# Performance work log

Measured on AMD Instinct MI355X. Metric: run time of the kernel, lower is better.

## Reference

```python
import jax, jax.numpy as jnp
import numpy as np


def setup_inputs() -> dict:
    key = jax.random.key(0)
    k1, k2 = jax.random.split(key)
    N, D, K = 262144, 64, 1024
    residual = jax.random.normal(k1, (N, D), dtype=jnp.float32)
    # nn.init.uniform_(codebook.weight, -1/K, 1/K)
    codebook = jax.random.uniform(k2, (K, D), dtype=jnp.float32,
                                  minval=-1.0 / K, maxval=1.0 / K)
    return {"residual": residual, "codebook": codebook}


def reference(residual, codebook):
    # squared L2 distances via ||a||^2 + ||b||^2 - 2 a.b (argmin-equivalent to
    # the broadcast (N,K,D) form, without materializing it)
    r2 = jnp.sum(residual * residual, axis=1, keepdims=True)        # (N, 1)
    c2 = jnp.sum(codebook * codebook, axis=1)[None, :]              # (1, K)
    dists = r2 + c2 - 2.0 * (residual @ codebook.T)                 # (N, K)
    codes = jnp.argmin(dists, axis=1)                               # (N,) int
    quantized = codebook[codes]                                     # (N, D)
    return quantized, codes
```

## Files before the change

kernel.cpp:

```cpp
#include <hip/hip_runtime.h>
#include <float.h>

#define D 64

typedef float f32x4 __attribute__((ext_vector_type(4)));
typedef _Float16 f16x8 __attribute__((ext_vector_type(8)));

__device__ __forceinline__ float np_sum_sq_64(const float* v) {
  float s[8];
#pragma unroll
  for (int j = 0; j < 8; ++j) s[j] = __fmul_rn(v[j], v[j]);
#pragma unroll
  for (int b = 1; b < 8; ++b) {
#pragma unroll
    for (int j = 0; j < 8; ++j)
      s[j] = __fadd_rn(s[j], __fmul_rn(v[8 * b + j], v[8 * b + j]));
  }
  float t01 = __fadd_rn(s[0], s[1]);
  float t23 = __fadd_rn(s[2], s[3]);
  float t45 = __fadd_rn(s[4], s[5]);
  float t67 = __fadd_rn(s[6], s[7]);
  return __fadd_rn(__fadd_rn(t01, t23), __fadd_rn(t45, t67));
}

__device__ __forceinline__ unsigned int pkh(float a, float b) {
  union { _Float16 h[2]; unsigned int u; } x;
  x.h[0] = (_Float16)a;
  x.h[1] = (_Float16)b;
  return x.u;
}

__global__ __launch_bounds__(64) void vq_prep(
    const float* __restrict__ cb, unsigned short* __restrict__ cbh,
    float4* __restrict__ cbT4, float* __restrict__ c2,
    unsigned int* __restrict__ counters, int K) {
  if (blockIdx.x == 0 && threadIdx.x == 0) { counters[0] = 0u; counters[1] = 0u; }
  int k = blockIdx.x * 64 + threadIdx.x;
  if (k >= K) return;
  float row[D];
  const float4* cp = (const float4*)(cb + (size_t)k * D);
#pragma unroll
  for (int i = 0; i < 16; ++i) {
    float4 v = cp[i];
    row[4 * i] = v.x; row[4 * i + 1] = v.y;
    row[4 * i + 2] = v.z; row[4 * i + 3] = v.w;
    cbT4[(size_t)i * K + k] = v;
    *(uint2*)(cbh + (size_t)k * D + 4 * i) =
        make_uint2(pkh(v.x * 1024.f, v.y * 1024.f),
                   pkh(v.z * 1024.f, v.w * 1024.f));
  }
  c2[k] = np_sum_sq_64(row);
}

__global__ __launch_bounds__(256, 3) void vq_screen(
    const float* __restrict__ residual, const float* __restrict__ codebook,
    const unsigned short* __restrict__ cbh, const float* __restrict__ c2,
    float* __restrict__ out_q, float* __restrict__ codes_f,
    unsigned int* __restrict__ counters, int* __restrict__ list,
    int N, int K) {
  __shared__ unsigned short smem[4096];
  __shared__ float srow[64];

  int tid = threadIdx.x;
  int rowbase = blockIdx.x * 64;

  float sr4[4];
#pragma unroll
  for (int jj = 0; jj < 4; ++jj) {
    int i = tid + 256 * jj;
    int r = i >> 4, d0 = (i & 15) * 4;
    float4 v = *(const float4*)(residual + (size_t)(rowbase + r) * D + d0);
    sr4[jj] = fabsf(v.x) + fabsf(v.y) + fabsf(v.z) + fabsf(v.w);
    int tile = r >> 4, rr = r & 15;
    int kblk = d0 >> 5, kk = d0 & 31;
    int lanep = rr + 16 * (kk >> 3);
    int off = ((tile * 2 + kblk) * 64 + lanep) * 8 + (kk & 7);
    *(uint2*)(smem + off) = make_uint2(pkh(v.x, v.y), pkh(v.z, v.w));
  }
#pragma unroll
  for (int jj = 0; jj < 4; ++jj) {
    float s = sr4[jj];
    s += __shfl_xor(s, 1, 64);
    s += __shfl_xor(s, 2, 64);
    s += __shfl_xor(s, 4, 64);
    s += __shfl_xor(s, 8, 64);
    sr4[jj] = s;
  }
  if ((tid & 15) == 0) {
#pragma unroll
    for (int jj = 0; jj < 4; ++jj) srow[(tid >> 4) + 16 * jj] = sr4[jj];
  }
  __syncthreads();

  int w = tid >> 6, lane = tid & 63;
  int lane15 = lane & 15, lq = lane >> 4;

  f16x8 ah[4][2];
#pragma unroll
  for (int t = 0; t < 4; ++t)
#pragma unroll
    for (int kb = 0; kb < 2; ++kb)
      ah[t][kb] = *(const f16x8*)(smem + ((t * 2 + kb) * 64 + lane) * 8);

  float m1[4][4], m2[4][4], m3[4][4];
#pragma unroll
  for (int t = 0; t < 4; ++t)
#pragma unroll
    for (int j = 0; j < 4; ++j) {
      m1[t][j] = FLT_MAX; m2[t][j] = FLT_MAX; m3[t][j] = FLT_MAX;
    }

  const unsigned short* ph = cbh + (size_t)(w * 16 + lane15) * D + lq * 8;
  const float* pc2 = c2 + (w * 16 + lane15);

  f16x8 B0a = *(const f16x8*)(ph);
  f16x8 B1a = *(const f16x8*)(ph + 32);
  float c2a = *pc2;
  ph += 64 * D; pc2 += 64;
  f16x8 B0b = *(const f16x8*)(ph);
  f16x8 B1b = *(const f16x8*)(ph + 32);
  float c2b = *pc2;

  unsigned int idb = (unsigned int)((w << 4) | lane15);
  for (int cc = 0; cc < 16; ++cc) {
    f16x8 ch0 = B0a, ch1 = B1a;
    float c2v = c2a;
    B0a = B0b; B1a = B1b; c2a = c2b;
    if (cc < 14) {
      ph += 64 * D; pc2 += 64;
      B0b = *(const f16x8*)(ph);
      B1b = *(const f16x8*)(ph + 32);
      c2b = *pc2;
    }

#pragma unroll
    for (int t = 0; t < 4; ++t) {
      f32x4 a = {0.f, 0.f, 0.f, 0.f};
      a = __builtin_amdgcn_mfma_f32_16x16x32_f16(ah[t][0], ch0, a, 0, 0, 0);
      a = __builtin_amdgcn_mfma_f32_16x16x32_f16(ah[t][1], ch1, a, 0, 0, 0);
#pragma unroll
      for (int j = 0; j < 4; ++j) {
        float s = __builtin_fmaf(-0.001953125f, a[j], c2v);
        float spf = __uint_as_float((__float_as_uint(s) & 0xFFFFFC00u) | idb);
        float o2 = m2[t][j];
        m3[t][j] = __builtin_amdgcn_fmed3f(o2, m3[t][j], spf);
        m2[t][j] = __builtin_amdgcn_fmed3f(m1[t][j], o2, spf);
        m1[t][j] = fminf(m1[t][j], spf);
      }
    }
    idb += 64u;
  }

#pragma unroll
  for (int dlt = 1; dlt < 16; dlt <<= 1) {
#pragma unroll
    for (int t = 0; t < 4; ++t)
#pragma unroll
      for (int j = 0; j < 4; ++j) {
        float a1 = m1[t][j], a2 = m2[t][j], a3 = m3[t][j];
        float b1 = __shfl_xor(a1, dlt, 64);
        float b2 = __shfl_xor(a2, dlt, 64);
        float b3 = __shfl_xor(a3, dlt, 64);
        m1[t][j] = fminf(a1, b1);
        m2[t][j] = fminf(fminf(fmaxf(a1, b1), a2), b2);
        m3[t][j] = fminf(fminf(fmaxf(a2, b1), fmaxf(a1, b2)), fminf(a3, b3));
      }
  }

  __syncthreads();
  float* red = (float*)smem;
  int* code_lds = ((int*)smem) + 768;
  if (lane15 == 0) {
#pragma unroll
    for (int t = 0; t < 4; ++t)
#pragma unroll
      for (int j = 0; j < 4; ++j) {
        int r = t * 16 + lq * 4 + j;
        int base = (w * 64 + r) * 3;
        red[base + 0] = m1[t][j];
        red[base + 1] = m2[t][j];
        red[base + 2] = m3[t][j];
      }
  }
  __syncthreads();
  if (tid < 64) {
    float a1 = red[tid * 3 + 0], a2 = red[tid * 3 + 1], a3 = red[tid * 3 + 2];
#pragma unroll
    for (int wv = 1; wv < 4; ++wv) {
      float b1 = red[(wv * 64 + tid) * 3 + 0];
      float b2 = red[(wv * 64 + tid) * 3 + 1];
      float b3 = red[(wv * 64 + tid) * 3 + 2];
      float n1 = fminf(a1, b1);
      float n2 = fminf(fminf(fmaxf(a1, b1), a2), b2);
      float n3 = fminf(fminf(fmaxf(a2, b1), fmaxf(a1, b2)), fminf(a3, b3));
      a1 = n1; a2 = n2; a3 = n3;
    }
    unsigned int u1 = __float_as_uint(a1);
    unsigned int u2 = __float_as_uint(a2);
    unsigned int u3 = __float_as_uint(a3);
    int ka = (int)(u1 & 1023u);
    float g1 = __uint_as_float(u1 & 0xFFFFFC00u);
    float g2 = __uint_as_float(u2 & 0xFFFFFC00u);
    float g3 = __uint_as_float(u3 & 0xFFFFFC00u);
    float margin = __builtin_fmaf(srow[tid], 4.6e-6f, 4.0e-5f);
    int row = rowbase + tid;
    code_lds[tid] = ka;
    float cf = (float)ka;
    if (g2 - g1 < margin) {
      if (g3 - g1 < margin) {
        unsigned int s = atomicAdd(counters + 0, 1u);
        list[s] = row;
      } else {
        unsigned int s = atomicAdd(counters + 1, 1u);
        list[N - 1 - (int)s] = row;
        cf = (float)(int)((unsigned int)ka | ((u2 & 1023u) << 10));
      }
    }
    codes_f[row] = cf;
  }
  __syncthreads();

  for (int e = tid; e < 4096; e += 256) {
    int r = e >> 6, d = e & 63;
    out_q[(size_t)rowbase * D + e] = codebook[((size_t)code_lds[r] << 6) + d];
  }
}

__global__ __launch_bounds__(256) void vq_pair(
    const float* __restrict__ residual, const float* __restrict__ codebook,
    const float* __restrict__ c2, float* __restrict__ codes_f,
    float* __restrict__ out_q, const unsigned int* __restrict__ counters,
    const int* __restrict__ list, int N) {
  unsigned int cnt = counters[1];
  for (unsigned int i = blockIdx.x * 256 + threadIdx.x; i < cnt;
       i += gridDim.x * 256) {
    int row = list[N - 1 - (int)i];
    int packed = (int)codes_f[row];
    int ka = packed & 1023, kb = packed >> 10;

    float r[D];
    const float4* rp = (const float4*)(residual + ((size_t)row << 6));
#pragma unroll
    for (int q = 0; q < 16; ++q) {
      float4 v = rp[q];
      r[4 * q] = v.x; r[4 * q + 1] = v.y; r[4 * q + 2] = v.z; r[4 * q + 3] = v.w;
    }
    float r2 = np_sum_sq_64(r);

    float da = 0.f, db = 0.f;
    const float4* ap = (const float4*)(codebook + ((size_t)ka << 6));
    const float4* bp = (const float4*)(codebook + ((size_t)kb << 6));
#pragma unroll
    for (int q = 0; q < 16; ++q) {
      float4 x = ap[q], y = bp[q];
      da = __fmaf_rn(r[4 * q + 0], x.x, da); db = __fmaf_rn(r[4 * q + 0], y.x, db);
      da = __fmaf_rn(r[4 * q + 1], x.y, da); db = __fmaf_rn(r[4 * q + 1], y.y, db);
      da = __fmaf_rn(r[4 * q + 2], x.z, da); db = __fmaf_rn(r[4 * q + 2], y.z, db);
      da = __fmaf_rn(r[4 * q + 3], x.w, da); db = __fmaf_rn(r[4 * q + 3], y.w, db);
    }
    float dista = __fsub_rn(__fadd_rn(r2, c2[ka]), __fmul_rn(2.0f, da));
    float distb = __fsub_rn(__fadd_rn(r2, c2[kb]), __fmul_rn(2.0f, db));
    bool bwin = (distb < dista) || (distb == dista && kb < ka);
    int win = bwin ? kb : ka;
    codes_f[row] = (float)win;
    if (bwin) {
      float4* oq = (float4*)(out_q + ((size_t)row << 6));
      const float4* cw = (const float4*)(codebook + ((size_t)win << 6));
#pragma unroll
      for (int q = 0; q < 16; ++q) oq[q] = cw[q];
    }
  }
}

__global__ __launch_bounds__(256) void vq_rescore(
    const float* __restrict__ residual, const float* __restrict__ codebook,
    const float4* __restrict__ cbT4, const float* __restrict__ c2,
    float* __restrict__ codes_f, float* __restrict__ out_q,
    const unsigned int* __restrict__ counters,
    const int* __restrict__ list, int K) {
  unsigned int cnt = counters[0];
  int w = threadIdx.x >> 6, lane = threadIdx.x & 63;
  unsigned int npairs = (cnt + 1) >> 1;
  for (unsigned int g = blockIdx.x * 4 + w; g < npairs; g += gridDim.x * 4) {
    int n0 = list[2 * g];
    bool two = (2 * g + 1 < cnt);
    int n1 = two ? list[2 * g + 1] : n0;

    float rl0 = residual[(size_t)n0 * D + lane];
    float rl1 = residual[(size_t)n1 * D + lane];

    int j = lane & 7;
    float x0 = __shfl(rl0, j, 64), x1 = __shfl(rl1, j, 64);
    float s0 = __fmul_rn(x0, x0), s1 = __fmul_rn(x1, x1);
#pragma unroll
    for (int b = 1; b < 8; ++b) {
      x0 = __shfl(rl0, 8 * b + j, 64);
      x1 = __shfl(rl1, 8 * b + j, 64);
      s0 = __fadd_rn(s0, __fmul_rn(x0, x0));
      s1 = __fadd_rn(s1, __fmul_rn(x1, x1));
    }
    s0 = __fadd_rn(s0, __shfl_xor(s0, 1, 64));
    s1 = __fadd_rn(s1, __shfl_xor(s1, 1, 64));
    s0 = __fadd_rn(s0, __shfl_xor(s0, 2, 64));
    s1 = __fadd_rn(s1, __shfl_xor(s1, 2, 64));
    s0 = __fadd_rn(s0, __shfl_xor(s0, 4, 64));
    s1 = __fadd_rn(s1, __shfl_xor(s1, 4, 64));
    float r2_0 = s0, r2_1 = s1;

    float m0[16], m1v[16];
#pragma unroll
    for (int ch = 0; ch < 16; ++ch) { m0[ch] = 0.f; m1v[ch] = 0.f; }

    for (int d4 = 0; d4 < 16; ++d4) {
      float a0 = __shfl(rl0, 4 * d4, 64), b0 = __shfl(rl0, 4 * d4 + 1, 64);
      float c0 = __shfl(rl0, 4 * d4 + 2, 64), e0 = __shfl(rl0, 4 * d4 + 3, 64);
      float a1 = __shfl(rl1, 4 * d4, 64), b1 = __shfl(rl1, 4 * d4 + 1, 64);
      float c1 = __shfl(rl1, 4 * d4 + 2, 64), e1 = __shfl(rl1, 4 * d4 + 3, 64);
      const float4* bp = cbT4 + (size_t)d4 * K + lane;
      float4 cbv[8];
#pragma unroll
      for (int h = 0; h < 2; ++h) {
#pragma unroll
        for (int q = 0; q < 8; ++q) cbv[q] = bp[(h * 8 + q) * 64];
#pragma unroll
        for (int q = 0; q < 8; ++q) {
          int ch = h * 8 + q;
          float4 c = cbv[q];
          float t0 = m0[ch], t1 = m1v[ch];
          t0 = __fmaf_rn(a0, c.x, t0); t1 = __fmaf_rn(a1, c.x, t1);
          t0 = __fmaf_rn(b0, c.y, t0); t1 = __fmaf_rn(b1, c.y, t1);
          t0 = __fmaf_rn(c0, c.z, t0); t1 = __fmaf_rn(c1, c.z, t1);
          t0 = __fmaf_rn(e0, c.w, t0); t1 = __fmaf_rn(e1, c.w, t1);
          m0[ch] = t0; m1v[ch] = t1;
        }
      }
    }

    float best0 = FLT_MAX, best1 = FLT_MAX;
    int bk0 = 0, bk1 = 0;
#pragma unroll
    for (int ch = 0; ch < 16; ++ch) {
      int code = ch * 64 + lane;
      float c2v = c2[code];
      float d0 = __fsub_rn(__fadd_rn(r2_0, c2v), __fmul_rn(2.0f, m0[ch]));
      float d1 = __fsub_rn(__fadd_rn(r2_1, c2v), __fmul_rn(2.0f, m1v[ch]));
      if (d0 < best0) { best0 = d0; bk0 = code; }
      if (d1 < best1) { best1 = d1; bk1 = code; }
    }
#pragma unroll
    for (int off = 32; off > 0; off >>= 1) {
      float ob = __shfl_down(best0, off, 64);
      int oi = __shfl_down(bk0, off, 64);
      if (ob < best0 || (ob == best0 && oi < bk0)) { best0 = ob; bk0 = oi; }
      ob = __shfl_down(best1, off, 64);
      oi = __shfl_down(bk1, off, 64);
      if (ob < best1 || (ob == best1 && oi < bk1)) { best1 = ob; bk1 = oi; }
    }
    int k0 = __shfl(bk0, 0, 64);
    int k1 = __shfl(bk1, 0, 64);
    if (lane == 0) codes_f[n0] = (float)k0;
    out_q[(size_t)n0 * D + lane] = codebook[((size_t)k0 << 6) + lane];
    if (two) {
      if (lane == 0) codes_f[n1] = (float)k1;
      out_q[(size_t)n1 * D + lane] = codebook[((size_t)k1 << 6) + lane];
    }
  }
}

extern "C" void kernel_launch(void* const* d_in, const int* in_sizes, int n_in,
                              void* d_out, int out_size, void* d_ws, size_t ws_size,
                              hipStream_t stream) {
  const float* residual = (const float*)d_in[0];
  const float* codebook = (const float*)d_in[1];
  int N = in_sizes[0] / D;
  int K = in_sizes[1] / D;

  float* out_q = (float*)d_out;
  float* codes_f = out_q + (size_t)N * D;

  char* ws = (char*)d_ws;
  float* c2 = (float*)ws;
  unsigned short* cbh = (unsigned short*)(ws + (size_t)K * 4);
  float4* cbT4 = (float4*)(ws + (size_t)K * 4 + (size_t)K * D * 2);
  unsigned int* counters =
      (unsigned int*)(ws + (size_t)K * 4 + (size_t)K * D * 2 + (size_t)K * D * 4);
  int* list = (int*)(counters + 2);

  vq_prep<<<(K + 63) / 64, 64, 0, stream>>>(codebook, cbh, cbT4, c2,
                                            counters, K);

  vq_screen<<<N / 64, 256, 0, stream>>>(residual, codebook, cbh, c2, out_q,
                                        codes_f, counters, list, N, K);

  vq_pair<<<512, 256, 0, stream>>>(residual, codebook, c2, codes_f, out_q,
                                   counters, list, N);

  vq_rescore<<<2048, 256, 0, stream>>>(residual, codebook, cbT4, c2, codes_f,
                                       out_q, counters, list, K);
}
```

Before: 245.6 us.

## Restructure VQ screen loop per row-tile, fold c2 into MFMA accumulator, raise occupancy

The screen kernel now processes one 16-row tile at a time in an outer non-unrolled loop, so it keeps only 4 running top-3 sets instead of 16. That cuts register pressure and allows the launch bound of 6 blocks per CU. The scaled negative codebook norm is precomputed and used as the MFMA accumulator's initial value, which removes the per-element FMA, and the top-3 tracking switches from min to max. The trade-off is that every tile re-streams the codebook from global/L2 memory four times, and the margin constants are rescaled to match the new scoring.

```diff
diff --git a/kernel.cpp b/kernel.cpp
--- a/kernel.cpp
+++ b/kernel.cpp
@@ -33,7 +33,7 @@
 __global__ __launch_bounds__(64) void vq_prep(
     const float* __restrict__ cb, unsigned short* __restrict__ cbh,
     float4* __restrict__ cbT4, float* __restrict__ c2,
-    unsigned int* __restrict__ counters, int K) {
+    float* __restrict__ c2n, unsigned int* __restrict__ counters, int K) {
   if (blockIdx.x == 0 && threadIdx.x == 0) { counters[0] = 0u; counters[1] = 0u; }
   int k = blockIdx.x * 64 + threadIdx.x;
   if (k >= K) return;
@@ -49,16 +49,20 @@
         make_uint2(pkh(v.x * 1024.f, v.y * 1024.f),
                    pkh(v.z * 1024.f, v.w * 1024.f));
   }
-  c2[k] = np_sum_sq_64(row);
-}
-
-__global__ __launch_bounds__(256, 3) void vq_screen(
+  float c2v = np_sum_sq_64(row);
+  c2[k] = c2v;
+  c2n[k] = -512.0f * c2v;
+}
+
+__global__ __launch_bounds__(256, 6) void vq_screen(
     const float* __restrict__ residual, const float* __restrict__ codebook,
-    const unsigned short* __restrict__ cbh, const float* __restrict__ c2,
+    const unsigned short* __restrict__ cbh, const float* __restrict__ c2n,
     float* __restrict__ out_q, float* __restrict__ codes_f,
     unsigned int* __restrict__ counters, int* __restrict__ list,
     int N, int K) {
   __shared__ unsigned short smem[4096];
+  __shared__ float red[768];
+  __shared__ int code_lds[64];
   __shared__ float srow[64];
 
   int tid = threadIdx.x;
@@ -95,93 +99,80 @@
   int w = tid >> 6, lane = tid & 63;
   int lane15 = lane & 15, lq = lane >> 4;
 
-  f16x8 ah[4][2];
-#pragma unroll
-  for (int t = 0; t < 4; ++t)
-#pragma unroll
-    for (int kb = 0; kb < 2; ++kb)
-      ah[t][kb] = *(const f16x8*)(smem + ((t * 2 + kb) * 64 + lane) * 8);
-
-  float m1[4][4], m2[4][4], m3[4][4];
-#pragma unroll
-  for (int t = 0; t < 4; ++t)
+#pragma unroll 1
+  for (int t = 0; t < 4; ++t) {
+    f16x8 ah0 = *(const f16x8*)(smem + ((t * 2 + 0) * 64 + lane) * 8);
+    f16x8 ah1 = *(const f16x8*)(smem + ((t * 2 + 1) * 64 + lane) * 8);
+
+    float m1[4], m2[4], m3[4];
 #pragma unroll
     for (int j = 0; j < 4; ++j) {
-      m1[t][j] = FLT_MAX; m2[t][j] = FLT_MAX; m3[t][j] = FLT_MAX;
-    }
-
-  const unsigned short* ph = cbh + (size_t)(w * 16 + lane15) * D + lq * 8;
-  const float* pc2 = c2 + (w * 16 + lane15);
-
-  f16x8 B0a = *(const f16x8*)(ph);
-  f16x8 B1a = *(const f16x8*)(ph + 32);
-  float c2a = *pc2;
-  ph += 64 * D; pc2 += 64;
-  f16x8 B0b = *(const f16x8*)(ph);
-  f16x8 B1b = *(const f16x8*)(ph + 32);
-  float c2b = *pc2;
-
-  unsigned int idb = (unsigned int)((w << 4) | lane15);
-  for (int cc = 0; cc < 16; ++cc) {
-    f16x8 ch0 = B0a, ch1 = B1a;
-    float c2v = c2a;
-    B0a = B0b; B1a = B1b; c2a = c2b;
-    if (cc < 14) {
-      ph += 64 * D; pc2 += 64;
-      B0b = *(const f16x8*)(ph);
-      B1b = *(const f16x8*)(ph + 32);
-      c2b = *pc2;
-    }
-
-#pragma unroll
-    for (int t = 0; t < 4; ++t) {
-      f32x4 a = {0.f, 0.f, 0.f, 0.f};
-      a = __builtin_amdgcn_mfma_f32_16x16x32_f16(ah[t][0], ch0, a, 0, 0, 0);
-      a = __builtin_amdgcn_mfma_f32_16x16x32_f16(ah[t][1], ch1, a, 0, 0, 0);
+      m1[j] = -FLT_MAX; m2[j] = -FLT_MAX; m3[j] = -FLT_MAX;
+    }
+
+    const unsigned short* ph = cbh + (size_t)(w * 16 + lane15) * D + lq * 8;
+    const float* pc2 = c2n + (w * 16 + lane15);
+
+    f16x8 B0a = *(const f16x8*)(ph);
+    f16x8 B1a = *(const f16x8*)(ph + 32);
+    float c2a = *pc2;
+    ph += 64 * D; pc2 += 64;
+    f16x8 B0b = *(const f16x8*)(ph);
+    f16x8 B1b = *(const f16x8*)(ph + 32);
+    float c2b = *pc2;
+
+    unsigned int idb = (unsigned int)((w << 4) | lane15);
+    for (int cc = 0; cc < 16; ++cc) {
+      f16x8 ch0 = B0a, ch1 = B1a;
+      float q = c2a;
+      B0a = B0b; B1a = B1b; c2a = c2b;
+      if (cc < 14) {
+        ph += 64 * D; pc2 += 64;
+        B0b = *(const f16x8*)(ph);
+        B1b = *(const f16x8*)(ph + 32);
+        c2b = *pc2;
+      }
+
+      f32x4 a = {q, q, q, q};
+      a = __builtin_amdgcn_mfma_f32_16x16x32_f16(ah0, ch0, a, 0, 0, 0);
+      a = __builtin_amdgcn_mfma_f32_16x16x32_f16(ah1, ch1, a, 0, 0, 0);
 #pragma unroll
       for (int j = 0; j < 4; ++j) {
-        float s = __builtin_fmaf(-0.001953125f, a[j], c2v);
-        float spf = __uint_as_float((__float_as_uint(s) & 0xFFFFFC00u) | idb);
-        float o2 = m2[t][j];
-        m3[t][j] = __builtin_amdgcn_fmed3f(o2, m3[t][j], spf);
-        m2[t][j] = __builtin_amdgcn_fmed3f(m1[t][j], o2, spf);
-        m1[t][j] = fminf(m1[t][j], spf);
-      }
-    }
-    idb += 64u;
-  }
-
-#pragma unroll
-  for (int dlt = 1; dlt < 16; dlt <<= 1) {
-#pragma unroll
-    for (int t = 0; t < 4; ++t)
+        float spf = __uint_as_float((__float_as_uint(a[j]) & 0xFFFFFC00u) | idb);
+        float o1 = m1[j], o2 = m2[j];
+        m3[j] = __builtin_amdgcn_fmed3f(o2, m3[j], spf);
+        m2[j] = __builtin_amdgcn_fmed3f(o1, o2, spf);
+        m1[j] = fmaxf(o1, spf);
+      }
+      idb += 64u;
+    }
+
+#pragma unroll
+    for (int dlt = 1; dlt < 16; dlt <<= 1) {
 #pragma unroll
       for (int j = 0; j < 4; ++j) {
-        float a1 = m1[t][j], a2 = m2[t][j], a3 = m3[t][j];
+        float a1 = m1[j], a2 = m2[j], a3 = m3[j];
         float b1 = __shfl_xor(a1, dlt, 64);
         float b2 = __shfl_xor(a2, dlt, 64);
         float b3 = __shfl_xor(a3, dlt, 64);
-        m1[t][j] = fminf(a1, b1);
-        m2[t][j] = fminf(fminf(fmaxf(a1, b1), a2), b2);
-        m3[t][j] = fminf(fminf(fmaxf(a2, b1), fmaxf(a1, b2)), fminf(a3, b3));
-      }
-  }
-
-  __syncthreads();
-  float* red = (float*)smem;
-  int* code_lds = ((int*)smem) + 768;
-  if (lane15 == 0) {
-#pragma unroll
-    for (int t = 0; t < 4; ++t)
+        m1[j] = fmaxf(a1, b1);
+        m2[j] = fmaxf(fminf(a1, b1), fmaxf(a2, b2));
+        m3[j] = fmaxf(fmaxf(fminf(a2, b1), fminf(a1, b2)), fmaxf(a3, b3));
+      }
+    }
+
+    if (lane15 == 0) {
 #pragma unroll
       for (int j = 0; j < 4; ++j) {
         int r = t * 16 + lq * 4 + j;
         int base = (w * 64 + r) * 3;
-        red[base + 0] = m1[t][j];
-        red[base + 1] = m2[t][j];
-        red[base + 2] = m3[t][j];
-      }
-  }
+        red[base + 0] = m1[j];
+        red[base + 1] = m2[j];
+        red[base + 2] = m3[j];
+      }
+    }
+  }
+
   __syncthreads();
   if (tid < 64) {
     float a1 = red[tid * 3 + 0], a2 = red[tid * 3 + 1], a3 = red[tid * 3 + 2];
@@ -190,9 +181,9 @@
       float b1 = red[(wv * 64 + tid) * 3 + 0];
       float b2 = red[(wv * 64 + tid) * 3 + 1];
       float b3 = red[(wv * 64 + tid) * 3 + 2];
-      float n1 = fminf(a1, b1);
-      float n2 = fminf(fminf(fmaxf(a1, b1), a2), b2);
-      float n3 = fminf(fminf(fmaxf(a2, b1), fmaxf(a1, b2)), fminf(a3, b3));
+      float n1 = fmaxf(a1, b1);
+      float n2 = fmaxf(fminf(a1, b1), fmaxf(a2, b2));
+      float n3 = fmaxf(fmaxf(fminf(a2, b1), fminf(a1, b2)), fmaxf(a3, b3));
       a1 = n1; a2 = n2; a3 = n3;
     }
     unsigned int u1 = __float_as_uint(a1);
@@ -202,12 +193,12 @@
     float g1 = __uint_as_float(u1 & 0xFFFFFC00u);
     float g2 = __uint_as_float(u2 & 0xFFFFFC00u);
     float g3 = __uint_as_float(u3 & 0xFFFFFC00u);
-    float margin = __builtin_fmaf(srow[tid], 4.6e-6f, 4.0e-5f);
+    float margin = __builtin_fmaf(srow[tid], 2.3552e-3f, 2.048e-2f);
     int row = rowbase + tid;
     code_lds[tid] = ka;
     float cf = (float)ka;
-    if (g2 - g1 < margin) {
-      if (g3 - g1 < margin) {
+    if (g1 - g2 < margin) {
+      if (g1 - g3 < margin) {
         unsigned int s = atomicAdd(counters + 0, 1u);
         list[s] = row;
       } else {
@@ -380,16 +371,17 @@
 
   char* ws = (char*)d_ws;
   float* c2 = (float*)ws;
-  unsigned short* cbh = (unsigned short*)(ws + (size_t)K * 4);
-  float4* cbT4 = (float4*)(ws + (size_t)K * 4 + (size_t)K * D * 2);
+  float* c2n = (float*)(ws + (size_t)K * 4);
+  unsigned short* cbh = (unsigned short*)(ws + (size_t)K * 8);
+  float4* cbT4 = (float4*)(ws + (size_t)K * 8 + (size_t)K * D * 2);
   unsigned int* counters =
-      (unsigned int*)(ws + (size_t)K * 4 + (size_t)K * D * 2 + (size_t)K * D * 4);
+      (unsigned int*)(ws + (size_t)K * 8 + (size_t)K * D * 2 + (size_t)K * D * 4);
   int* list = (int*)(counters + 2);
 
-  vq_prep<<<(K + 63) / 64, 64, 0, stream>>>(codebook, cbh, cbT4, c2,
+  vq_prep<<<(K + 63) / 64, 64, 0, stream>>>(codebook, cbh, cbT4, c2, c2n,
                                             counters, K);
 
-  vq_screen<<<N / 64, 256, 0, stream>>>(residual, codebook, cbh, c2, out_q,
+  vq_screen<<<N / 64, 256, 0, stream>>>(residual, codebook, cbh, c2n, out_q,
                                         codes_f, counters, list, N, K);
 
   vq_pair<<<512, 256, 0, stream>>>(residual, codebook, c2, codes_f, out_q,
```

New measurement: 746.5 us. 204% more time.
